# Kernel tuning notes

Hardware: AMD Instinct MI355X
Metric: run time of the kernel (lower is better)

The kernel has to match this reference:

```python
import jax, jax.numpy as jnp
import numpy as np

ROUTING_ITER = 2
EPS = 1e-8


def squash(s, axis):
    # s * ||s||^2 / (1 + ||s||^2) / ||s||
    sq = jnp.sum(s * s, axis=axis, keepdims=True)
    return s * (sq / (1.0 + sq)) / jnp.sqrt(sq + EPS)


def setup_inputs() -> dict:
    key = jax.random.key(0)
    k1, k2 = jax.random.split(key)
    B, N_in, d_in = 64, 2048, 16
    J, D = 32, 16  # num_capsule, dim_capsule
    x = jax.random.normal(k1, (B, N_in, 1, d_in), dtype=jnp.float32)
    weight = jax.random.normal(k2, (1, N_in, J, D, d_in), dtype=jnp.float32) * 0.05
    return {"x": x, "weight": weight}


def reference(x, weight):
    # x: [B, N_in, 1, d_in]; weight: [1, N_in, J, D, d_in]
    # prediction vectors u[b,i,j,:] = W[i,j] @ x[b,i]
    u = jnp.einsum('ijde,bie->bijd', weight[0], x[:, :, 0, :])  # [B,N_in,J,D]
    B, N_in, J, D = u.shape

    # dynamic routing on stop_gradient(u)
    u_sg = jax.lax.stop_gradient(u)
    b = jnp.zeros((B, N_in, J, 1), dtype=u.dtype)
    for _ in range(ROUTING_ITER):
        c = jax.nn.softmax(b, axis=2)                      # [B,N_in,J,1]
        s = jnp.sum(u_sg * c, axis=1, keepdims=True)       # [B,1,J,D]
        v = squash(s, axis=2)                              # squash over capsule axis (faithful)
        b = b + jnp.sum(u_sg * v, axis=-1, keepdims=True)  # [B,N_in,J,1]

    c = jax.nn.softmax(b, axis=2)
    s = jnp.sum(u * c, axis=1)  # [B,J,D]
    return squash(s, axis=-1)
```

## Files before the change

### kernel.cpp

```cpp
#include <hip/hip_runtime.h>

typedef __attribute__((ext_vector_type(8))) short short8;
typedef __attribute__((ext_vector_type(4))) float f32x4;
typedef __attribute__((ext_vector_type(2))) float f32x2;
typedef __attribute__((ext_vector_type(4))) unsigned int uint4v;
typedef unsigned short u16;

#define NI 2048

__device__ __forceinline__ unsigned int packbf2(float a, float b){
  unsigned int ua = __float_as_uint(a), ub = __float_as_uint(b);
  unsigned int ra = (ua + 0x7FFFu + ((ua >> 16) & 1u)) >> 16;
  unsigned int rb = (ub + 0x7FFFu + ((ub >> 16) & 1u)) & 0xFFFF0000u;
  return ra | rb;
}
__device__ __forceinline__ float bflo(unsigned int p){ return __uint_as_float(p << 16); }
__device__ __forceinline__ float bfhi(unsigned int p){ return __uint_as_float(p & 0xFFFF0000u); }

__device__ __forceinline__ uint4v cvt8(const f32x4& a, const f32x4& b){
  uint4v p = { packbf2(a.x, a.y), packbf2(a.z, a.w),
               packbf2(b.x, b.y), packbf2(b.z, b.w) };
  return p;
}

__device__ __forceinline__ void gl_lds16(const void* g, void* l){
  __builtin_amdgcn_global_load_lds(
      (const __attribute__((address_space(1))) unsigned int*)g,
      (__attribute__((address_space(3))) unsigned int*)l, 16, 0, 0);
}


#define FUSED_SMEM 150656

template<int MODE>
__device__ __forceinline__ void pass_phase(
    const u16* __restrict__ sW, const u16* __restrict__ sX,
    float* __restrict__ sSumA, float* __restrict__ sSumB,
    const float* __restrict__ Sv1, const float* __restrict__ qv1,
    const float* __restrict__ Sv2, const float* __restrict__ qv2,
    float* __restrict__ partials, int blk, int t)
{
  const int w = t >> 6, lane = t & 63;
  const int wtile = w & 1, jhalf = (w >> 1) & 1, bh = w >> 2;
  const int lq = lane >> 4, lb = lane & 15, qs = lq & 1;
  const int bg = bh * 32 + wtile * 16 + lb;
  const short8 zero8 = {0,0,0,0,0,0,0,0};
  const f32x4 zf4 = {0.f,0.f,0.f,0.f};

  f32x4 acc[16];
  #pragma unroll
  for (int tj = 0; tj < 16; ++tj) acc[tj] = zf4;

  unsigned int vpl[16], vph[16];
  if constexpr (MODE >= 1){
    f32x4 qa = *(const f32x4*)(qv1 + bg * 16 + lq * 4);
    f32x4 fa;
    fa.x = qa.x / ((1.f + qa.x) * sqrtf(qa.x + 1e-8f));
    fa.y = qa.y / ((1.f + qa.y) * sqrtf(qa.y + 1e-8f));
    fa.z = qa.z / ((1.f + qa.z) * sqrtf(qa.z + 1e-8f));
    fa.w = qa.w / ((1.f + qa.w) * sqrtf(qa.w + 1e-8f));
    f32x4 fb = zf4;
    if constexpr (MODE == 2){
      f32x4 qb = *(const f32x4*)(qv2 + bg * 16 + lq * 4);
      fb.x = qb.x / ((1.f + qb.x) * sqrtf(qb.x + 1e-8f));
      fb.y = qb.y / ((1.f + qb.y) * sqrtf(qb.y + 1e-8f));
      fb.z = qb.z / ((1.f + qb.z) * sqrtf(qb.z + 1e-8f));
      fb.w = qb.w / ((1.f + qb.w) * sqrtf(qb.w + 1e-8f));
    }
    #pragma unroll
    for (int tj = 0; tj < 16; ++tj){
      int jd = (jhalf * 16 + tj) * 16 + lq * 4;
      f32x4 sv = *(const f32x4*)(Sv1 + bg * 512 + jd);
      f32x4 v;
      v.x = sv.x * fa.x; v.y = sv.y * fa.y; v.z = sv.z * fa.z; v.w = sv.w * fa.w;
      if constexpr (MODE == 2){
        f32x4 s2 = *(const f32x4*)(Sv2 + bg * 512 + jd);
        v.x += s2.x * fb.x; v.y += s2.y * fb.y; v.z += s2.z * fb.z; v.w += s2.w * fb.w;
      }
      vpl[tj] = packbf2(v.x, v.y);
      vph[tj] = packbf2(v.z, v.w);
    }
  }

  if constexpr (MODE == 0){
    const int rsel = lq >> 1;
    #pragma unroll
    for (int s = 0; s < 4; ++s){
      const u16* wrow = sW + (size_t)(2 * s + rsel) * 8192;
      const u16* xrow = sX + (size_t)(2 * s + rsel) * 1024;
      short8 bfrag = *(const short8*)(xrow + bg * 16 + qs * 8);
      #pragma unroll
      for (int tj = 0; tj < 16; ++tj){
        int j = jhalf * 16 + tj;
        short8 afrag = *(const short8*)(wrow + j * 256 + lb * 16 + qs * 8);
        acc[tj] = __builtin_amdgcn_mfma_f32_16x16x32_bf16(afrag, bfrag, acc[tj], 0, 0, 0);
      }
    }
  } else {
    for (int s = 0; s < 8; ++s){
      const u16* wrow = sW + (size_t)s * 8192;
      const u16* xrow = sX + (size_t)s * 1024;
      short8 bl8 = *(const short8*)(xrow + bg * 16 + qs * 8);
      short8 bfrag = (lq < 2) ? bl8 : zero8;
      f32x4 ut[16];
      float e[16];
      float ps = 0.f;
      #pragma unroll
      for (int tj = 0; tj < 16; ++tj){
        int j = jhalf * 16 + tj;
        short8 afrag = *(const short8*)(wrow + j * 256 + lb * 16 + qs * 8);
        ut[tj] = __builtin_amdgcn_mfma_f32_16x16x32_bf16(afrag, bfrag, zf4, 0, 0, 0);
        float p = ut[tj].x * bflo(vpl[tj]) + ut[tj].y * bfhi(vpl[tj])
                + ut[tj].z * bflo(vph[tj]) + ut[tj].w * bfhi(vph[tj]);
        p += __shfl_xor(p, 16, 64);
        p += __shfl_xor(p, 32, 64);
        e[tj] = __expf(p);
        ps += e[tj];
      }
      float* sS = (s & 1) ? sSumB : sSumA;
      if (lane < 16) sS[w * 16 + lane] = ps;
      __syncthreads();
      float inv = 1.0f / (ps + sS[(w ^ 2) * 16 + lb]);
      #pragma unroll
      for (int tj = 0; tj < 16; ++tj){
        float c = e[tj] * inv;
        acc[tj].x += c * ut[tj].x;
        acc[tj].y += c * ut[tj].y;
        acc[tj].z += c * ut[tj].z;
        acc[tj].w += c * ut[tj].w;
      }
    }
  }

  float* dst = partials + ((size_t)blk * 8 + (size_t)w) * 4096 + (size_t)lane * 64;
  #pragma unroll
  for (int tj = 0; tj < 16; ++tj) *(f32x4*)(dst + tj * 4) = acc[tj];
}

__device__ __forceinline__ void reduce_phase(
    const float* __restrict__ partials, float* __restrict__ S,
    float* __restrict__ qbuf, float scale, float* __restrict__ sRed,
    int blk, int t)
{
  const int o = blk * 128 + (t & 127);
  const int quarter = t >> 7;
  const float* src = partials + (size_t)quarter * 64 * 32768 + (size_t)o;
  float s = 0.f;
  #pragma unroll 16
  for (int p = 0; p < 64; ++p) s += src[(size_t)p * 32768];
  sRed[t] = s;
  __syncthreads();
  if (t < 128){
    float tot = ((sRed[t] + sRed[t + 128]) + (sRed[t + 256] + sRed[t + 384])) * scale;
    const int bh = o >> 14, wd = (o >> 12) & 3, ln = (o >> 6) & 63, k = o & 63;
    const int b = bh * 32 + (wd & 1) * 16 + (ln & 15);
    const int j = (wd >> 1) * 16 + (k >> 2);
    const int d = ((ln >> 4) << 2) + (k & 3);
    S[b * 512 + j * 16 + d] = tot;
    if (qbuf) atomicAdd(qbuf + b * 16 + d, tot * tot);
  }
  __syncthreads();
}

__global__ __launch_bounds__(512, 2)
void caps_fused(const float* __restrict__ X, const float* __restrict__ W,
                unsigned int* __restrict__ gcnt,
                float* __restrict__ qb1, float* __restrict__ qb2,
                float* __restrict__ S1, float* __restrict__ S2, float* __restrict__ S3,
                float* __restrict__ partials, float* __restrict__ out)
{
  extern __shared__ __align__(16) char smem[];
  u16* sW = (u16*)smem;
  u16* sX = (u16*)(smem + 131072);
  float* sSumA = (float*)(smem + 147456);
  float* sSumB = sSumA + 128;
  float* sRed  = sSumB + 128;
  float* sq    = sRed + 512;

  const int t = threadIdx.x;
  const int blk = blockIdx.x;
  const size_t i0 = (size_t)blk * 8;

  {
    const float* wsrc = W + i0 * 8192;
    #pragma unroll
    for (int k = 0; k < 16; ++k){
      int idx = k * 4096 + t * 8;
      f32x4 a = *(const f32x4*)(wsrc + idx);
      f32x4 b = *(const f32x4*)(wsrc + idx + 4);
      *(uint4v*)(sW + idx) = cvt8(a, b);
    }
    int r = t >> 6, b = t & 63;
    const float* xs = X + ((size_t)b * NI + i0 + (size_t)r) * 16;
    f32x4 a0 = *(const f32x4*)(xs);
    f32x4 a1 = *(const f32x4*)(xs + 4);
    f32x4 a2 = *(const f32x4*)(xs + 8);
    f32x4 a3 = *(const f32x4*)(xs + 12);
    *(uint4v*)(sX + t * 16)     = cvt8(a0, a1);
    *(uint4v*)(sX + t * 16 + 8) = cvt8(a2, a3);
  }
  __syncthreads();

  unsigned int gen = 0;
  auto gridsync = [&](){
    ++gen;
    __syncthreads();
    if (t == 0){
      __threadfence();
      __hip_atomic_fetch_add(gcnt, 1u, __ATOMIC_ACQ_REL, __HIP_MEMORY_SCOPE_AGENT);
      const unsigned int target = gen * 256u;
      while (__hip_atomic_load(gcnt, __ATOMIC_ACQUIRE, __HIP_MEMORY_SCOPE_AGENT) < target)
        __builtin_amdgcn_s_sleep(2);
      __threadfence();
    }
    __syncthreads();
  };

  pass_phase<0>(sW, sX, sSumA, sSumB, nullptr, nullptr, nullptr, nullptr, partials, blk, t);
  gridsync();
  reduce_phase(partials, S1, qb1, 1.0f / 32.0f, sRed, blk, t);
  gridsync();

  pass_phase<1>(sW, sX, sSumA, sSumB, S1, qb1, nullptr, nullptr, partials, blk, t);
  gridsync();
  reduce_phase(partials, S2, qb2, 1.0f, sRed, blk, t);
  gridsync();

  pass_phase<2>(sW, sX, sSumA, sSumB, S1, qb1, S2, qb2, partials, blk, t);
  gridsync();
  reduce_phase(partials, S3, nullptr, 1.0f, sRed, blk, t);
  gridsync();

  if (blk < 64){
    if (t < 32) sq[t] = 0.f;
    __syncthreads();
    float s0 = 0.f, s1 = 0.f;
    if (t < 256){
      s0 = S3[blk * 512 + t];
      s1 = S3[blk * 512 + 256 + t];
      atomicAdd(&sq[t >> 4], s0 * s0);
      atomicAdd(&sq[(t + 256) >> 4], s1 * s1);
    }
    __syncthreads();
    if (t < 256){
      float a = sq[t >> 4], c = sq[(t + 256) >> 4];
      out[blk * 512 + t]       = s0 * (a / ((1.f + a) * sqrtf(a + 1e-8f)));
      out[blk * 512 + 256 + t] = s1 * (c / ((1.f + c) * sqrtf(c + 1e-8f)));
    }
  }
}


__global__ __launch_bounds__(256)
void caps_prep(const float* __restrict__ W, const float* __restrict__ X,
               u16* __restrict__ Wb, u16* __restrict__ Xb)
{
  const int bid = blockIdx.x;
  if (bid < 8192){
    size_t base = (size_t)bid * 2048 + (size_t)threadIdx.x * 8;
    f32x4 a = *(const f32x4*)(W + base);
    f32x4 b = *(const f32x4*)(W + base + 4);
    *(uint4v*)(Wb + base) = cvt8(a, b);
  } else {
    int p = (bid - 8192) * 256 + threadIdx.x;
    int i = p >> 6, b = p & 63;
    const float* src = X + ((size_t)b * NI + i) * 16;
    f32x4 a0 = *(const f32x4*)(src);
    f32x4 a1 = *(const f32x4*)(src + 4);
    f32x4 a2 = *(const f32x4*)(src + 8);
    f32x4 a3 = *(const f32x4*)(src + 12);
    *(uint4v*)(Xb + (size_t)p * 16)     = cvt8(a0, a1);
    *(uint4v*)(Xb + (size_t)p * 16 + 8) = cvt8(a2, a3);
  }
}

template<int MODE>
__global__ __launch_bounds__(256, 2)
void caps_pass_f(const u16* __restrict__ Wb,
                 const u16* __restrict__ Xb,
                 const float* __restrict__ vbuf,
                 float* __restrict__ partials, int CI)
{
  constexpr int WR = (MODE == 0) ? 2 : 1;
  __shared__ __align__(16) u16 sW[2][WR * 8192];
  __shared__ __align__(16) u16 sX[2][WR * 512];
  __shared__ float sSum[4][16];

  const int t     = threadIdx.x;
  const int w     = t >> 6;
  const int lane  = t & 63;
  const int wtile = w & 1;
  const int jhalf = w >> 1;
  const int lq    = lane >> 4;
  const int lb    = lane & 15;
  const int q1    = lq & 1;
  const int bhalf = blockIdx.x & 1;
  const int iblk  = blockIdx.x >> 1;
  const int bloc  = wtile * 16 + lb;
  const int bg    = bhalf * 32 + bloc;
  const size_t i0 = (size_t)iblk * (size_t)CI;

  const short8 zero8 = {0,0,0,0,0,0,0,0};
  const f32x4  zf4   = {0.f,0.f,0.f,0.f};

  f32x4 acc[16];
  #pragma unroll
  for (int tj = 0; tj < 16; ++tj) acc[tj] = zf4;

  unsigned int vpl[16], vph[16];
  if constexpr (MODE == 1){
    #pragma unroll
    for (int tj = 0; tj < 16; ++tj){
      f32x4 v = *(const f32x4*)(&vbuf[bg * 512 + (jhalf * 16 + tj) * 16 + lq * 4]);
      vpl[tj] = packbf2(v.x, v.y);
      vph[tj] = packbf2(v.z, v.w);
    }
  }

  auto stage = [&](int nb, size_t irow){
    #pragma unroll
    for (int rr = 0; rr < WR; ++rr){
      const u16* src = Wb + (irow + rr) * 8192 + (size_t)(w * 4) * 512;
      u16* dst = &sW[nb][rr * 8192 + w * 4 * 512];
      #pragma unroll
      for (int r = 0; r < 4; ++r)
        gl_lds16(src + r * 512 + lane * 8, dst + r * 512);
    }
    if (w >= 4 - WR){
      int rr = w - (4 - WR);
      gl_lds16(Xb + ((irow + rr) * 64 + (size_t)bhalf * 32) * 16 + lane * 8,
               &sX[nb][rr * 512]);
    }
  };

  const int NSTEP = CI / WR;
  stage(0, i0);
  __syncthreads();

  for (int s = 0; s < NSTEP; ++s){
    const int buf = s & 1;
    if (s + 1 < NSTEP) stage(buf ^ 1, i0 + (size_t)(s + 1) * WR);

    if constexpr (MODE == 0){
      const int rsel = lq >> 1;
      short8 bfrag = *(const short8*)(&sX[buf][rsel * 512 + bloc * 16 + q1 * 8]);
      #pragma unroll
      for (int tj = 0; tj < 16; ++tj){
        int j = jhalf * 16 + tj;
        short8 afrag = *(const short8*)(&sW[buf][rsel * 8192 + j * 256 + lb * 16 + q1 * 8]);
        acc[tj] = __builtin_amdgcn_mfma_f32_16x16x32_bf16(afrag, bfrag, acc[tj], 0, 0, 0);
      }
    } else {
      short8 bl8 = *(const short8*)(&sX[buf][bloc * 16 + q1 * 8]);
      short8 bfrag = (lq < 2) ? bl8 : zero8;
      f32x4 ut[16];
      float e[16];
      float ps = 0.f;
      #pragma unroll
      for (int tj = 0; tj < 16; ++tj){
        int j = jhalf * 16 + tj;
        short8 al8 = *(const short8*)(&sW[buf][j * 256 + lb * 16 + q1 * 8]);
        short8 afrag = (lq < 2) ? al8 : zero8;
        ut[tj] = __builtin_amdgcn_mfma_f32_16x16x32_bf16(afrag, bfrag, zf4, 0, 0, 0);
        float p = ut[tj].x * bflo(vpl[tj]) + ut[tj].y * bfhi(vpl[tj])
                + ut[tj].z * bflo(vph[tj]) + ut[tj].w * bfhi(vph[tj]);
        p += __shfl_xor(p, 16, 64);
        p += __shfl_xor(p, 32, 64);
        e[tj] = __expf(p);
        ps += e[tj];
      }
      if (lane < 16) sSum[w][lane] = ps;
      __syncthreads();
      float inv = 1.0f / (ps + sSum[w ^ 2][lb]);
      #pragma unroll
      for (int tj = 0; tj < 16; ++tj){
        float c = e[tj] * inv;
        acc[tj].x += c * ut[tj].x;
        acc[tj].y += c * ut[tj].y;
        acc[tj].z += c * ut[tj].z;
        acc[tj].w += c * ut[tj].w;
      }
    }
    __syncthreads();
  }

  float* dst = partials + ((size_t)blockIdx.x * 4 + (size_t)w) * 4096 + (size_t)lane * 64;
  #pragma unroll
  for (int tj = 0; tj < 16; ++tj) *(f32x4*)(dst + tj * 4) = acc[tj];
}

template<int MODE>
__global__ __launch_bounds__(256)
void caps_pass_legacy(const float* __restrict__ Wg, const float* __restrict__ Xg,
                      const float* __restrict__ vbuf, float* __restrict__ partials, int CI)
{
  __shared__ __align__(16) unsigned short sW[2][8192];
  __shared__ __align__(16) unsigned int   sXd[2][256];
  __shared__ float sLog[(MODE == 1) ? (32 * 33) : 4];
  const int t = threadIdx.x, w = t >> 6, lane = t & 63;
  const int wtile = w & 1, jhalf = w >> 1, lq = lane >> 4, lb = lane & 15, q1 = lq & 1;
  const int bhalf = blockIdx.x & 1, iblk = blockIdx.x >> 1;
  const int bloc = wtile * 16 + lb, bg = bhalf * 32 + bloc;
  const size_t i0 = (size_t)iblk * (size_t)CI;
  const short8 zero8 = {0,0,0,0,0,0,0,0};
  const f32x4 zf4 = {0.f,0.f,0.f,0.f};
  f32x4 acc[16];
  #pragma unroll
  for (int tj = 0; tj < 16; ++tj) acc[tj] = zf4;
  unsigned int vpl[16], vph[16];
  if constexpr (MODE == 1){
    #pragma unroll
    for (int tj = 0; tj < 16; ++tj){
      f32x4 v = *(const f32x4*)(&vbuf[bg * 512 + (jhalf * 16 + tj) * 16 + lq * 4]);
      vpl[tj] = packbf2(v.x, v.y); vph[tj] = packbf2(v.z, v.w);
    }
  }
  {
    const float* wsrc = Wg + i0 * 8192;
    #pragma unroll
    for (int r = 0; r < 4; ++r){
      int c = r * 256 + t;
      f32x4 a = *(const f32x4*)(&wsrc[c * 8]);
      f32x4 b = *(const f32x4*)(&wsrc[c * 8 + 4]);
      *(uint4v*)(&sW[0][c * 8]) = cvt8(a, b);
    }
    int bidx = bhalf * 32 + (t >> 3), e2 = t & 7;
    f32x2 xv = *(const f32x2*)(&Xg[((size_t)bidx * NI + i0) * 16 + e2 * 2]);
    sXd[0][t] = packbf2(xv.x, xv.y);
  }
  __syncthreads();
  for (int s = 0; s < CI; ++s){
    const int buf = s & 1;
    f32x4 wpa[4], wpb[4]; f32x2 xp;
    const bool more = (s + 1 < CI);
    if (more){
      const float* wsrc = Wg + (i0 + (size_t)(s + 1)) * 8192;
      #pragma unroll
      for (int r = 0; r < 4; ++r){
        int c = r * 256 + t;
        wpa[r] = *(const f32x4*)(&wsrc[c * 8]);
        wpb[r] = *(const f32x4*)(&wsrc[c * 8 + 4]);
      }
      int bidx = bhalf * 32 + (t >> 3), e2 = t & 7;
      xp = *(const f32x2*)(&Xg[((size_t)bidx * NI + i0 + s + 1) * 16 + e2 * 2]);
    }
    const unsigned short* xrow = (const unsigned short*)&sXd[buf][0];
    short8 bl8 = *(const short8*)(&xrow[bloc * 16 + q1 * 8]);
    short8 bfrag = (lq < 2) ? bl8 : zero8;
    if constexpr (MODE == 0){
      #pragma unroll
      for (int tj = 0; tj < 16; ++tj){
        int j = jhalf * 16 + tj;
        short8 al8 = *(const short8*)(&sW[buf][j * 256 + lb * 16 + q1 * 8]);
        short8 afrag = (lq < 2) ? al8 : zero8;
        acc[tj] = __builtin_amdgcn_mfma_f32_16x16x32_bf16(afrag, bfrag, acc[tj], 0, 0, 0);
      }
    } else {
      #pragma unroll
      for (int tj = 0; tj < 16; ++tj){
        int j = jhalf * 16 + tj;
        short8 al8 = *(const short8*)(&sW[buf][j * 256 + lb * 16 + q1 * 8]);
        short8 afrag = (lq < 2) ? al8 : zero8;
        f32x4 u = __builtin_amdgcn_mfma_f32_16x16x32_bf16(afrag, bfrag, zf4, 0, 0, 0);
        float p = u.x * bflo(vpl[tj]) + u.y * bfhi(vpl[tj])
                + u.z * bflo(vph[tj]) + u.w * bfhi(vph[tj]);
        p += __shfl_xor(p, 16, 64);
        p += __shfl_xor(p, 32, 64);
        if (lane < 16) sLog[bloc * 33 + j] = p;
      }
      __syncthreads();
      const float* logrow = &sLog[bloc * 33];
      float ssum = 0.f;
      #pragma unroll
      for (int jj = 0; jj < 32; ++jj) ssum += __expf(logrow[jj]);
      float inv = 1.0f / ssum;
      #pragma unroll
      for (int tj = 0; tj < 16; ++tj){
        int j = jhalf * 16 + tj;
        short8 al8 = *(const short8*)(&sW[buf][j * 256 + lb * 16 + q1 * 8]);
        short8 afrag = (lq < 2) ? al8 : zero8;
        f32x4 u = __builtin_amdgcn_mfma_f32_16x16x32_bf16(afrag, bfrag, zf4, 0, 0, 0);
        float c = __expf(logrow[j]) * inv;
        acc[tj].x += c * u.x; acc[tj].y += c * u.y;
        acc[tj].z += c * u.z; acc[tj].w += c * u.w;
      }
    }
    if (more){
      const int nb = buf ^ 1;
      #pragma unroll
      for (int r = 0; r < 4; ++r){
        int c = r * 256 + t;
        *(uint4v*)(&sW[nb][c * 8]) = cvt8(wpa[r], wpb[r]);
      }
      sXd[nb][t] = packbf2(xp.x, xp.y);
    }
    __syncthreads();
  }
  float* dst = partials + ((size_t)blockIdx.x * 4 + (size_t)w) * 4096 + (size_t)lane * 64;
  #pragma unroll
  for (int tj = 0; tj < 16; ++tj) *(f32x4*)(dst + tj * 4) = acc[tj];
}

template<int NBLK>
__global__ __launch_bounds__(128)
void caps_reduce(const float* __restrict__ partials, float* __restrict__ S_buf, float scale)
{
  const int T = blockIdx.x * 128 + threadIdx.x;
  float s0 = 0.f, s1 = 0.f, s2 = 0.f, s3 = 0.f;
  #pragma unroll
  for (int bl = 0; bl < NBLK; bl += 4){
    s0 += partials[(size_t)(bl + 0) * 32768 + T];
    s1 += partials[(size_t)(bl + 1) * 32768 + T];
    s2 += partials[(size_t)(bl + 2) * 32768 + T];
    s3 += partials[(size_t)(bl + 3) * 32768 + T];
  }
  float s = ((s0 + s1) + (s2 + s3)) * scale;
  const int bhalf = T >> 14, w = (T >> 12) & 3, l = (T >> 6) & 63, k = T & 63;
  const int b  = bhalf * 32 + (w & 1) * 16 + (l & 15);
  const int jd = ((w >> 1) * 16 + (k >> 2)) * 16 + ((l >> 4) << 2) + (k & 3);
  S_buf[b * 512 + jd] = s;
}

__global__ __launch_bounds__(256)
void caps_squash_j(const float* __restrict__ S, const float* __restrict__ vprev,
                   float* __restrict__ vout)
{
  const int b = blockIdx.x, t = threadIdx.x;
  __shared__ float sq[16];
  if (t < 16) sq[t] = 0.f;
  __syncthreads();
  float s0 = S[b * 512 + t], s1 = S[b * 512 + 256 + t];
  atomicAdd(&sq[t & 15], s0 * s0 + s1 * s1);
  __syncthreads();
  float q = sq[t & 15];
  float f = q / ((1.f + q) * sqrtf(q + 1e-8f));
  float v0 = s0 * f, v1 = s1 * f;
  if (vprev){ v0 += vprev[b * 512 + t]; v1 += vprev[b * 512 + 256 + t]; }
  vout[b * 512 + t] = v0;
  vout[b * 512 + 256 + t] = v1;
}

__global__ __launch_bounds__(256)
void caps_squash_d(const float* __restrict__ S, float* __restrict__ out)
{
  const int b = blockIdx.x, t = threadIdx.x;
  __shared__ float sq[32];
  if (t < 32) sq[t] = 0.f;
  __syncthreads();
  float s0 = S[b * 512 + t], s1 = S[b * 512 + 256 + t];
  atomicAdd(&sq[t >> 4], s0 * s0);
  atomicAdd(&sq[(t + 256) >> 4], s1 * s1);
  __syncthreads();
  float q0 = sq[t >> 4], q1 = sq[(t + 256) >> 4];
  out[b * 512 + t]       = s0 * q0 / ((1.f + q0) * sqrtf(q0 + 1e-8f));
  out[b * 512 + 256 + t] = s1 * q1 / ((1.f + q1) * sqrtf(q1 + 1e-8f));
}

extern "C" void kernel_launch(void* const* d_in, const int* in_sizes, int n_in,
                              void* d_out, int out_size, void* d_ws, size_t ws_size,
                              hipStream_t stream)
{
  const float* X = (const float*)d_in[0];
  const float* W = (const float*)d_in[1];
  float* wsf = (float*)d_ws;

  const size_t OF_Q1   = 64;
  const size_t OF_Q2   = OF_Q1 + 1024;
  const size_t OF_S1   = OF_Q2 + 1024;
  const size_t OF_S2   = OF_S1 + 32768;
  const size_t OF_S3   = OF_S2 + 32768;
  const size_t OF_PART = OF_S3 + 32768;
  const size_t FUSED_FLOATS = OF_PART + (size_t)256 * 32768;

  static int fused_ok = -1;
  if (fused_ok < 0){
    fused_ok = 0;
    hipFuncSetAttribute(reinterpret_cast<const void*>(caps_fused),
                        hipFuncAttributeMaxDynamicSharedMemorySize, FUSED_SMEM);
    int dev = 0, ncu = 0, nb = 0;
    hipGetDevice(&dev);
    hipDeviceGetAttribute(&ncu, hipDeviceAttributeMultiprocessorCount, dev);
    hipError_t e = hipOccupancyMaxActiveBlocksPerMultiprocessor(
        &nb, caps_fused, 512, (size_t)FUSED_SMEM);
    if (e == hipSuccess && nb >= 1 && ncu >= 256) fused_ok = 1;
  }

  if (fused_ok == 1 && ws_size >= FUSED_FLOATS * 4){
    hipMemsetAsync(d_ws, 0, (64 + 1024 + 1024) * 4, stream);
    caps_fused<<<dim3(256), dim3(512), FUSED_SMEM, stream>>>(
        X, W, (unsigned int*)wsf, wsf + OF_Q1, wsf + OF_Q2,
        wsf + OF_S1, wsf + OF_S2, wsf + OF_S3, wsf + OF_PART, (float*)d_out);
    return;
  }

  const size_t FP = (size_t)256 * 32768;
  const size_t WB_ELE = (size_t)NI * 8192, XB_ELE = (size_t)NI * 64 * 16;
  const size_t need_full = (FP + 3 * 32768) * 4 + (WB_ELE + XB_ELE) * 2;

  if (ws_size >= need_full){
    float* partials = wsf;
    float* sbuf = wsf + FP;
    float* v1   = sbuf + 32768;
    float* v12  = v1 + 32768;
    u16* Wb = (u16*)(v12 + 32768);
    u16* Xb = Wb + WB_ELE;

    caps_prep<<<dim3(8704), dim3(256), 0, stream>>>(W, X, Wb, Xb);

    caps_pass_f<0><<<dim3(512), dim3(256), 0, stream>>>(Wb, Xb, nullptr, partials, 8);
    caps_reduce<256><<<dim3(256), dim3(128), 0, stream>>>(partials, sbuf, 1.0f / 32.0f);
    caps_squash_j<<<dim3(64), dim3(256), 0, stream>>>(sbuf, nullptr, v1);

    caps_pass_f<1><<<dim3(512), dim3(256), 0, stream>>>(Wb, Xb, v1, partials, 8);
    caps_reduce<256><<<dim3(256), dim3(128), 0, stream>>>(partials, sbuf, 1.0f);
    caps_squash_j<<<dim3(64), dim3(256), 0, stream>>>(sbuf, v1, v12);

    caps_pass_f<1><<<dim3(512), dim3(256), 0, stream>>>(Wb, Xb, v12, partials, 8);
    caps_reduce<256><<<dim3(256), dim3(128), 0, stream>>>(partials, sbuf, 1.0f);
    caps_squash_d<<<dim3(64), dim3(256), 0, stream>>>(sbuf, (float*)d_out);
  } else {
    int NBI = 256;
    auto need = [](int nb){ return ((size_t)nb * 32768 + 3 * 32768) * 4; };
    if (ws_size < need(256)){
      if      (ws_size >= need(64)) NBI = 64;
      else if (ws_size >= need(16)) NBI = 16;
      else                          NBI = 4;
    }
    const int CI = NI / NBI;
    float* partials = wsf;
    float* sbuf = wsf + (size_t)NBI * 32768;
    float* v1   = sbuf + 32768;
    float* v12  = v1 + 32768;
    auto reduce = [&](float scale){
      if      (NBI == 256) caps_reduce<256><<<dim3(256), dim3(128), 0, stream>>>(partials, sbuf, scale);
      else if (NBI ==  64) caps_reduce< 64><<<dim3(256), dim3(128), 0, stream>>>(partials, sbuf, scale);
      else if (NBI ==  16) caps_reduce< 16><<<dim3(256), dim3(128), 0, stream>>>(partials, sbuf, scale);
      else                 caps_reduce<  4><<<dim3(256), dim3(128), 0, stream>>>(partials, sbuf, scale);
    };
    caps_pass_legacy<0><<<dim3(2 * NBI), dim3(256), 0, stream>>>(W, X, nullptr, partials, CI);
    reduce(1.0f / 32.0f);
    caps_squash_j<<<dim3(64), dim3(256), 0, stream>>>(sbuf, nullptr, v1);
    caps_pass_legacy<1><<<dim3(2 * NBI), dim3(256), 0, stream>>>(W, X, v1, partials, CI);
    reduce(1.0f);
    caps_squash_j<<<dim3(64), dim3(256), 0, stream>>>(sbuf, v1, v12);
    caps_pass_legacy<1><<<dim3(2 * NBI), dim3(256), 0, stream>>>(W, X, v12, partials, CI);
    reduce(1.0f);
    caps_squash_d<<<dim3(64), dim3(256), 0, stream>>>(sbuf, (float*)d_out);
  }
}
```

Measured before the change: 232.1 us.

## Relax grid barrier fences, use coherent atomic loads/stores, and fold final squash norms into reduce

Replaces the acquire/release fences and threadfences in the software grid barrier with relaxed atomics. All cross-block data (partials, S, q buffers) now goes through agent-scope relaxed atomic 64-bit loads and stores, which keep it coherent without full cache flushes. The reduce phase now has each thread sum two adjacent outputs over 32 partials with 8 groups. The final reduce also accumulates per-(b,j) squared norms, so the epilogue skips the shared-memory norm pass. The intent is to cut barrier fence and cache-maintenance cost; correctness now relies on relaxed ordering being sufficient under the memory model.

```diff
diff --git a/kernel.cpp b/kernel.cpp
--- a/kernel.cpp
+++ b/kernel.cpp
@@ -5,6 +5,7 @@
 typedef __attribute__((ext_vector_type(2))) float f32x2;
 typedef __attribute__((ext_vector_type(4))) unsigned int uint4v;
 typedef unsigned short u16;
+typedef unsigned long long u64;
 
 #define NI 2048
 
@@ -29,8 +30,29 @@
       (__attribute__((address_space(3))) unsigned int*)l, 16, 0, 0);
 }
 
-
-#define FUSED_SMEM 150656
+union F2U { f32x2 f; u64 u; };
+
+__device__ __forceinline__ void st_u64_coh(float* p, float a, float b){
+  F2U v; v.f.x = a; v.f.y = b;
+  __hip_atomic_store((u64*)p, v.u, __ATOMIC_RELAXED, __HIP_MEMORY_SCOPE_AGENT);
+}
+__device__ __forceinline__ f32x2 ld_f2_coh(const float* p){
+  F2U v; v.u = __hip_atomic_load((const u64*)p, __ATOMIC_RELAXED, __HIP_MEMORY_SCOPE_AGENT);
+  return v.f;
+}
+__device__ __forceinline__ f32x4 ld_f4_coh(const float* p){
+  f32x2 a = ld_f2_coh(p), b = ld_f2_coh(p + 2);
+  f32x4 r; r.x = a.x; r.y = a.y; r.z = b.x; r.w = b.y; return r;
+}
+__device__ __forceinline__ void st_f4_coh(float* p, const f32x4& v){
+  st_u64_coh(p, v.x, v.y); st_u64_coh(p + 2, v.z, v.w);
+}
+__device__ __forceinline__ float ld_f_coh(const float* p){
+  return __hip_atomic_load((const float*)p, __ATOMIC_RELAXED, __HIP_MEMORY_SCOPE_AGENT);
+}
+
+
+#define FUSED_SMEM 152576
 
 template<int MODE>
 __device__ __forceinline__ void pass_phase(
@@ -53,7 +75,7 @@
 
   unsigned int vpl[16], vph[16];
   if constexpr (MODE >= 1){
-    f32x4 qa = *(const f32x4*)(qv1 + bg * 16 + lq * 4);
+    f32x4 qa = ld_f4_coh(qv1 + bg * 16 + lq * 4);
     f32x4 fa;
     fa.x = qa.x / ((1.f + qa.x) * sqrtf(qa.x + 1e-8f));
     fa.y = qa.y / ((1.f + qa.y) * sqrtf(qa.y + 1e-8f));
@@ -61,7 +83,7 @@
     fa.w = qa.w / ((1.f + qa.w) * sqrtf(qa.w + 1e-8f));
     f32x4 fb = zf4;
     if constexpr (MODE == 2){
-      f32x4 qb = *(const f32x4*)(qv2 + bg * 16 + lq * 4);
+      f32x4 qb = ld_f4_coh(qv2 + bg * 16 + lq * 4);
       fb.x = qb.x / ((1.f + qb.x) * sqrtf(qb.x + 1e-8f));
       fb.y = qb.y / ((1.f + qb.y) * sqrtf(qb.y + 1e-8f));
       fb.z = qb.z / ((1.f + qb.z) * sqrtf(qb.z + 1e-8f));
@@ -70,11 +92,11 @@
     #pragma unroll
     for (int tj = 0; tj < 16; ++tj){
       int jd = (jhalf * 16 + tj) * 16 + lq * 4;
-      f32x4 sv = *(const f32x4*)(Sv1 + bg * 512 + jd);
+      f32x4 sv = ld_f4_coh(Sv1 + bg * 512 + jd);
       f32x4 v;
       v.x = sv.x * fa.x; v.y = sv.y * fa.y; v.z = sv.z * fa.z; v.w = sv.w * fa.w;
       if constexpr (MODE == 2){
-        f32x4 s2 = *(const f32x4*)(Sv2 + bg * 512 + jd);
+        f32x4 s2 = ld_f4_coh(Sv2 + bg * 512 + jd);
         v.x += s2.x * fb.x; v.y += s2.y * fb.y; v.z += s2.z * fb.z; v.w += s2.w * fb.w;
       }
       vpl[tj] = packbf2(v.x, v.y);
@@ -134,30 +156,48 @@
 
   float* dst = partials + ((size_t)blk * 8 + (size_t)w) * 4096 + (size_t)lane * 64;
   #pragma unroll
-  for (int tj = 0; tj < 16; ++tj) *(f32x4*)(dst + tj * 4) = acc[tj];
+  for (int tj = 0; tj < 16; ++tj) st_f4_coh(dst + tj * 4, acc[tj]);
 }
 
 __device__ __forceinline__ void reduce_phase(
     const float* __restrict__ partials, float* __restrict__ S,
-    float* __restrict__ qbuf, float scale, float* __restrict__ sRed,
-    int blk, int t)
-{
-  const int o = blk * 128 + (t & 127);
-  const int quarter = t >> 7;
-  const float* src = partials + (size_t)quarter * 64 * 32768 + (size_t)o;
-  float s = 0.f;
-  #pragma unroll 16
-  for (int p = 0; p < 64; ++p) s += src[(size_t)p * 32768];
-  sRed[t] = s;
-  __syncthreads();
-  if (t < 128){
-    float tot = ((sRed[t] + sRed[t + 128]) + (sRed[t + 256] + sRed[t + 384])) * scale;
-    const int bh = o >> 14, wd = (o >> 12) & 3, ln = (o >> 6) & 63, k = o & 63;
+    float* __restrict__ qbd, float* __restrict__ qbj,
+    float scale, float* __restrict__ sRed, int blk, int t)
+{
+  const int pr = t & 63;
+  const int dg = t >> 6;
+  const int o  = blk * 128 + pr * 2;
+  const float* src = partials + (size_t)dg * 32 * 32768 + (size_t)o;
+  float a0 = 0.f, a1 = 0.f;
+  #pragma unroll 8
+  for (int p = 0; p < 32; ++p){
+    f32x2 v = ld_f2_coh(src + (size_t)p * 32768);
+    a0 += v.x; a1 += v.y;
+  }
+  sRed[t * 2]     = a0;
+  sRed[t * 2 + 1] = a1;
+  __syncthreads();
+  if (t < 64){
+    float t0 = 0.f, t1 = 0.f;
+    #pragma unroll
+    for (int g = 0; g < 8; ++g){
+      t0 += sRed[(g * 64 + t) * 2];
+      t1 += sRed[(g * 64 + t) * 2 + 1];
+    }
+    t0 *= scale; t1 *= scale;
+    const int oo = blk * 128 + t * 2;
+    const int bh = oo >> 14, wd = (oo >> 12) & 3, ln = (oo >> 6) & 63, k = oo & 63;
     const int b = bh * 32 + (wd & 1) * 16 + (ln & 15);
     const int j = (wd >> 1) * 16 + (k >> 2);
     const int d = ((ln >> 4) << 2) + (k & 3);
-    S[b * 512 + j * 16 + d] = tot;
-    if (qbuf) atomicAdd(qbuf + b * 16 + d, tot * tot);
+    st_u64_coh(S + b * 512 + j * 16 + d, t0, t1);
+    if (qbd){
+      atomicAdd(qbd + b * 16 + d,     t0 * t0);
+      atomicAdd(qbd + b * 16 + d + 1, t1 * t1);
+    }
+    if (qbj){
+      atomicAdd(qbj + b * 32 + j, t0 * t0 + t1 * t1);
+    }
   }
   __syncthreads();
 }
@@ -166,6 +206,7 @@
 void caps_fused(const float* __restrict__ X, const float* __restrict__ W,
                 unsigned int* __restrict__ gcnt,
                 float* __restrict__ qb1, float* __restrict__ qb2,
+                float* __restrict__ qb3,
                 float* __restrict__ S1, float* __restrict__ S2, float* __restrict__ S3,
                 float* __restrict__ partials, float* __restrict__ out)
 {
@@ -175,7 +216,6 @@
   float* sSumA = (float*)(smem + 147456);
   float* sSumB = sSumA + 128;
   float* sRed  = sSumB + 128;
-  float* sq    = sRed + 512;
 
   const int t = threadIdx.x;
   const int blk = blockIdx.x;
@@ -206,47 +246,33 @@
     ++gen;
     __syncthreads();
     if (t == 0){
-      __threadfence();
-      __hip_atomic_fetch_add(gcnt, 1u, __ATOMIC_ACQ_REL, __HIP_MEMORY_SCOPE_AGENT);
+      __hip_atomic_fetch_add(gcnt, 1u, __ATOMIC_RELAXED, __HIP_MEMORY_SCOPE_AGENT);
       const unsigned int target = gen * 256u;
-      while (__hip_atomic_load(gcnt, __ATOMIC_ACQUIRE, __HIP_MEMORY_SCOPE_AGENT) < target)
-        __builtin_amdgcn_s_sleep(2);
-      __threadfence();
+      while (__hip_atomic_load(gcnt, __ATOMIC_RELAXED, __HIP_MEMORY_SCOPE_AGENT) < target)
+        __builtin_amdgcn_s_sleep(8);
     }
     __syncthreads();
   };
 
   pass_phase<0>(sW, sX, sSumA, sSumB, nullptr, nullptr, nullptr, nullptr, partials, blk, t);
   gridsync();
-  reduce_phase(partials, S1, qb1, 1.0f / 32.0f, sRed, blk, t);
+  reduce_phase(partials, S1, qb1, nullptr, 1.0f / 32.0f, sRed, blk, t);
   gridsync();
 
   pass_phase<1>(sW, sX, sSumA, sSumB, S1, qb1, nullptr, nullptr, partials, blk, t);
   gridsync();
-  reduce_phase(partials, S2, qb2, 1.0f, sRed, blk, t);
+  reduce_phase(partials, S2, qb2, nullptr, 1.0f, sRed, blk, t);
   gridsync();
 
   pass_phase<2>(sW, sX, sSumA, sSumB, S1, qb1, S2, qb2, partials, blk, t);
   gridsync();
-  reduce_phase(partials, S3, nullptr, 1.0f, sRed, blk, t);
+  reduce_phase(partials, S3, nullptr, qb3, 1.0f, sRed, blk, t);
   gridsync();
 
   if (blk < 64){
-    if (t < 32) sq[t] = 0.f;
-    __syncthreads();
-    float s0 = 0.f, s1 = 0.f;
-    if (t < 256){
-      s0 = S3[blk * 512 + t];
-      s1 = S3[blk * 512 + 256 + t];
-      atomicAdd(&sq[t >> 4], s0 * s0);
-      atomicAdd(&sq[(t + 256) >> 4], s1 * s1);
-    }
-    __syncthreads();
-    if (t < 256){
-      float a = sq[t >> 4], c = sq[(t + 256) >> 4];
-      out[blk * 512 + t]       = s0 * (a / ((1.f + a) * sqrtf(a + 1e-8f)));
-      out[blk * 512 + 256 + t] = s1 * (c / ((1.f + c) * sqrtf(c + 1e-8f)));
-    }
+    float s = ld_f_coh(S3 + blk * 512 + t);
+    float q = ld_f_coh(qb3 + blk * 32 + (t >> 4));
+    out[blk * 512 + t] = s * (q / ((1.f + q) * sqrtf(q + 1e-8f)));
   }
 }
 
@@ -566,7 +592,8 @@
 
   const size_t OF_Q1   = 64;
   const size_t OF_Q2   = OF_Q1 + 1024;
-  const size_t OF_S1   = OF_Q2 + 1024;
+  const size_t OF_Q3   = OF_Q2 + 1024;
+  const size_t OF_S1   = OF_Q3 + 2048;
   const size_t OF_S2   = OF_S1 + 32768;
   const size_t OF_S3   = OF_S2 + 32768;
   const size_t OF_PART = OF_S3 + 32768;
@@ -586,9 +613,10 @@
   }
 
   if (fused_ok == 1 && ws_size >= FUSED_FLOATS * 4){
-    hipMemsetAsync(d_ws, 0, (64 + 1024 + 1024) * 4, stream);
+    hipMemsetAsync(d_ws, 0, (64 + 1024 + 1024 + 2048) * 4, stream);
     caps_fused<<<dim3(256), dim3(512), FUSED_SMEM, stream>>>(
-        X, W, (unsigned int*)wsf, wsf + OF_Q1, wsf + OF_Q2,
+        X, W, (unsigned int*)wsf,
+        wsf + OF_Q1, wsf + OF_Q2, wsf + OF_Q3,
         wsf + OF_S1, wsf + OF_S2, wsf + OF_S3, wsf + OF_PART, (float*)d_out);
     return;
   }
```

New measurement: 233.7 us. No clear change (+0.7%).
